# Kernel tuning notes

Hardware: AMD Instinct MI355X
Metric: run time of the kernel (lower is better)

Reference implementation:

```python
import jax, jax.numpy as jnp
import numpy as np

L, V, C, H, T_MAX, FF = 8, 50257, 1024, 16, 1024, 4096
DH = C // H
EPS = 1e-5


def setup_inputs() -> dict:
    key = jax.random.key(0)
    ks = jax.random.split(key, 16)
    s = 0.02
    inp = {
        "idx": jax.random.randint(ks[0], (2, 1024), 0, V, dtype=jnp.int32),
        "tok_emb": jax.random.normal(ks[1], (V, C), jnp.float32) * s,
        "pos_emb": jax.random.normal(ks[2], (T_MAX, C), jnp.float32) * s,
        "qkv_w": jax.random.normal(ks[3], (L, C, 3 * C), jnp.float32) * s,
        "qkv_b": jnp.zeros((L, 3 * C), jnp.float32),
        "out_w": jax.random.normal(ks[4], (L, C, C), jnp.float32) * s,
        "out_b": jnp.zeros((L, C), jnp.float32),
        "ln1_s": jnp.ones((L, C), jnp.float32),
        "ln1_b": jnp.zeros((L, C), jnp.float32),
        "ln2_s": jnp.ones((L, C), jnp.float32),
        "ln2_b": jnp.zeros((L, C), jnp.float32),
        "ffn_w1": jax.random.normal(ks[5], (L, C, FF), jnp.float32) * s,
        "ffn_b1": jnp.zeros((L, FF), jnp.float32),
        "ffn_w2": jax.random.normal(ks[6], (L, FF, C), jnp.float32) * s,
        "ffn_b2": jnp.zeros((L, C), jnp.float32),
        "lnf_s": jnp.ones((C,), jnp.float32),
        "lnf_b": jnp.zeros((C,), jnp.float32),
    }
    return inp


def _layernorm(x, scale, bias):
    m = jnp.mean(x, axis=-1, keepdims=True)
    v = jnp.mean(jnp.square(x - m), axis=-1, keepdims=True)
    return (x - m) * jax.lax.rsqrt(v + EPS) * scale + bias


def reference(idx, tok_emb, pos_emb, qkv_w, qkv_b, out_w, out_b,
              ln1_s, ln1_b, ln2_s, ln2_b,
              ffn_w1, ffn_b1, ffn_w2, ffn_b2, lnf_s, lnf_b):
    B, T = idx.shape
    x = tok_emb[idx] + pos_emb[:T]          # [B,T,C]
    causal = jnp.tril(jnp.ones((T, T), bool))  # [T,T]
    scale = 1.0 / np.sqrt(DH)

    def block(x, p):
        qw, qb, ow, ob, l1s, l1b, l2s, l2b, w1, b1, w2, b2 = p
        h = _layernorm(x, l1s, l1b)
        qkv = h @ qw + qb                    # [B,T,3C]
        q, k, v = jnp.split(qkv, 3, axis=-1)
        q = q.reshape(B, T, H, DH).transpose(0, 2, 1, 3)  # [B,H,T,Dh]
        k = k.reshape(B, T, H, DH).transpose(0, 2, 1, 3)
        v = v.reshape(B, T, H, DH).transpose(0, 2, 1, 3)
        scores = jnp.einsum('bhqd,bhkd->bhqk', q, k) * scale
        scores = jnp.where(causal, scores, -jnp.inf)
        w = jax.nn.softmax(scores, axis=-1)
        o = jnp.einsum('bhqk,bhkd->bhqd', w, v)
        o = o.transpose(0, 2, 1, 3).reshape(B, T, C)
        x = x + (o @ ow + ob)
        h2 = _layernorm(x, l2s, l2b)
        x = x + (jax.nn.gelu(h2 @ w1 + b1, approximate=False) @ w2 + b2)
        return x, None

    params = (qkv_w, qkv_b, out_w, out_b, ln1_s, ln1_b, ln2_s, ln2_b,
              ffn_w1, ffn_b1, ffn_w2, ffn_b2)
    x, _ = jax.lax.scan(block, x, params)
    x = _layernorm(x, lnf_s, lnf_b)
    logits = x @ tok_emb.T                   # tied head, no bias
    return logits
```

## Files before the change

kernel.cpp:

```cpp
#include <hip/hip_runtime.h>
#include <hip/hip_bf16.h>

#define NL 8
#define NV 50257
#define NC 1024
#define NH 16
#define NT 1024
#define NFF 4096
#define NB 2
#define NM (NB*NT)

typedef __attribute__((ext_vector_type(8))) short bf16x8;
typedef __attribute__((ext_vector_type(4))) float f32x4;

__device__ __forceinline__ unsigned short f2bf(float f) {
    union { float f; unsigned u; } a; a.f = f;
    unsigned r = a.u + 0x7FFFu + ((a.u >> 16) & 1u);
    return (unsigned short)(r >> 16);
}

__device__ __forceinline__ void gload16(const unsigned short* g, unsigned short* l) {
    __builtin_amdgcn_global_load_lds(
        (const __attribute__((address_space(1))) unsigned int*)g,
        (__attribute__((address_space(3))) unsigned int*)l,
        16, 0, 0);
}

__global__ __launch_bounds__(256) void embed_kernel(
    const int* __restrict__ idx, const float* __restrict__ te,
    const float* __restrict__ pe, float* __restrict__ x) {
    int row = blockIdx.x;
    int t = row & (NT - 1);
    int id = idx[row];
    const float4 a = reinterpret_cast<const float4*>(te + (size_t)id * NC)[threadIdx.x];
    const float4 b = reinterpret_cast<const float4*>(pe + (size_t)t * NC)[threadIdx.x];
    float4 o; o.x = a.x + b.x; o.y = a.y + b.y; o.z = a.z + b.z; o.w = a.w + b.w;
    reinterpret_cast<float4*>(x + (size_t)row * NC)[threadIdx.x] = o;
}

__global__ __launch_bounds__(256) void cvt_bf16_kernel(
    const float* __restrict__ in, unsigned short* __restrict__ out, size_t n4) {
    size_t i = (size_t)blockIdx.x * 256 + threadIdx.x;
    if (i >= n4) return;
    float4 v = reinterpret_cast<const float4*>(in)[i];
    uint2 u;
    u.x = (unsigned)f2bf(v.x) | ((unsigned)f2bf(v.y) << 16);
    u.y = (unsigned)f2bf(v.z) | ((unsigned)f2bf(v.w) << 16);
    reinterpret_cast<uint2*>(out)[i] = u;
}

__global__ __launch_bounds__(256) void wtrans_kernel(
    const float* __restrict__ W, unsigned short* __restrict__ Wt, int K, int N) {
    __shared__ float tile[32][33];
    int n0 = blockIdx.x * 32, k0 = blockIdx.y * 32;
    int tx = threadIdx.x, ty = threadIdx.y;
#pragma unroll
    for (int i = 0; i < 4; ++i)
        tile[ty + i * 8][tx] = W[(size_t)(k0 + ty + i * 8) * N + n0 + tx];
    __syncthreads();
#pragma unroll
    for (int i = 0; i < 4; ++i)
        Wt[(size_t)(n0 + ty + i * 8) * K + k0 + tx] = f2bf(tile[tx][ty + i * 8]);
}

__global__ __launch_bounds__(256) void ln_kernel(
    const float* __restrict__ x, const float* __restrict__ gam,
    const float* __restrict__ bet, unsigned short* __restrict__ out) {
    __shared__ float red[4];
    int row = blockIdx.x, tid = threadIdx.x;
    const float4 v = reinterpret_cast<const float4*>(x + (size_t)row * NC)[tid];
    float s = v.x + v.y + v.z + v.w;
#pragma unroll
    for (int m = 32; m >= 1; m >>= 1) s += __shfl_xor(s, m, 64);
    if ((tid & 63) == 0) red[tid >> 6] = s;
    __syncthreads();
    float mean = (red[0] + red[1] + red[2] + red[3]) * (1.0f / NC);
    __syncthreads();
    float dx = v.x - mean, dy = v.y - mean, dz = v.z - mean, dw = v.w - mean;
    float q = dx * dx + dy * dy + dz * dz + dw * dw;
#pragma unroll
    for (int m = 32; m >= 1; m >>= 1) q += __shfl_xor(q, m, 64);
    if ((tid & 63) == 0) red[tid >> 6] = q;
    __syncthreads();
    float var = (red[0] + red[1] + red[2] + red[3]) * (1.0f / NC);
    float rstd = rsqrtf(var + 1e-5f);
    int c = tid * 4;
    const float4 g4 = reinterpret_cast<const float4*>(gam)[tid];
    const float4 b4 = reinterpret_cast<const float4*>(bet)[tid];
    uint2 u;
    u.x = (unsigned)f2bf(dx * rstd * g4.x + b4.x) |
          ((unsigned)f2bf(dy * rstd * g4.y + b4.y) << 16);
    u.y = (unsigned)f2bf(dz * rstd * g4.z + b4.z) |
          ((unsigned)f2bf(dw * rstd * g4.w + b4.w) << 16);
    reinterpret_cast<uint2*>(out + (size_t)row * NC + c)[0] = u;
}

template<int ACT, bool BIAS, bool OUTBF16, bool NEDGE, bool ATOMIC>
__global__ __launch_bounds__(256) void gemm_kernel(
    const unsigned short* __restrict__ A, const unsigned short* __restrict__ Bt,
    const float* __restrict__ bias, void* __restrict__ Cout,
    int N, int K, int ldc, int ksub) {
    __shared__ unsigned short As[128 * 32];
    __shared__ unsigned short Bs[128 * 32];
    const int tid = threadIdx.x;
    const int lane = tid & 63;
    const int wave = tid >> 6;
    const int wm = wave >> 1, wn = wave & 1;
    const int lr = lane & 15, lg = lane >> 4;
    const int m0 = blockIdx.x * 128, n0 = blockIdx.y * 128;
    const int kbeg = blockIdx.z * ksub, kend = kbeg + ksub;

    const int r0 = tid >> 2;
    const int c0 = (tid & 3) * 8;
    int bn0 = n0 + r0, bn1 = n0 + r0 + 64;
    if (NEDGE) { bn0 = min(bn0, N - 1); bn1 = min(bn1, N - 1); }
    const unsigned short* Ag0 = A + (size_t)(m0 + r0) * K + c0;
    const unsigned short* Ag1 = A + (size_t)(m0 + r0 + 64) * K + c0;
    const unsigned short* Bg0 = Bt + (size_t)bn0 * K + c0;
    const unsigned short* Bg1 = Bt + (size_t)bn1 * K + c0;
    unsigned short* Al0 = As + wave * 512;
    unsigned short* Al1 = As + 2048 + wave * 512;
    unsigned short* Bl0 = Bs + wave * 512;
    unsigned short* Bl1 = Bs + 2048 + wave * 512;

    const f32x4 zero4 = {0.0f, 0.0f, 0.0f, 0.0f};
    f32x4 acc[4][4];
#pragma unroll
    for (int i = 0; i < 4; ++i)
#pragma unroll
        for (int j = 0; j < 4; ++j) acc[i][j] = zero4;

    for (int k0 = kbeg; k0 < kend; k0 += 32) {
        __syncthreads();
        gload16(Ag0 + k0, Al0);
        gload16(Ag1 + k0, Al1);
        gload16(Bg0 + k0, Bl0);
        gload16(Bg1 + k0, Bl1);
        __syncthreads();
        bf16x8 af[4], bfr[4];
#pragma unroll
        for (int f = 0; f < 4; ++f) {
            af[f]  = *reinterpret_cast<const bf16x8*>(As + (wm * 64 + f * 16 + lr) * 32 + lg * 8);
            bfr[f] = *reinterpret_cast<const bf16x8*>(Bs + (wn * 64 + f * 16 + lr) * 32 + lg * 8);
        }
#pragma unroll
        for (int i = 0; i < 4; ++i)
#pragma unroll
            for (int j = 0; j < 4; ++j)
                acc[i][j] = __builtin_amdgcn_mfma_f32_16x16x32_bf16(af[i], bfr[j], acc[i][j], 0, 0, 0);
    }

#pragma unroll
    for (int i = 0; i < 4; ++i) {
#pragma unroll
        for (int j = 0; j < 4; ++j) {
            int col = n0 + wn * 64 + j * 16 + lr;
            if (NEDGE && col >= N) continue;
            float bv = (BIAS && kbeg == 0) ? bias[col] : 0.0f;
#pragma unroll
            for (int r = 0; r < 4; ++r) {
                int row = m0 + wm * 64 + i * 16 + lg * 4 + r;
                float v = acc[i][j][r] + bv;
                if (ACT == 1) v = 0.5f * v * (1.0f + erff(v * 0.70710678118654752f));
                if (ATOMIC) {
                    atomicAdd(reinterpret_cast<float*>(Cout) + (size_t)row * ldc + col, v);
                } else if (OUTBF16) {
                    reinterpret_cast<unsigned short*>(Cout)[(size_t)row * ldc + col] = f2bf(v);
                } else {
                    reinterpret_cast<float*>(Cout)[(size_t)row * ldc + col] = v;
                }
            }
        }
    }
}

__global__ __launch_bounds__(256) void vtrans_kernel(
    const unsigned short* __restrict__ qkv, unsigned short* __restrict__ vt) {
    __shared__ unsigned short tile[32][33];
    int bh = blockIdx.z; int b = bh >> 4, h = bh & 15;
    int t0 = blockIdx.x * 32, d0 = blockIdx.y * 32;
    int tx = threadIdx.x, ty = threadIdx.y;
#pragma unroll
    for (int i = 0; i < 4; ++i)
        tile[ty + i * 8][tx] =
            qkv[(size_t)(b * NT + t0 + ty + i * 8) * 3072 + 2048 + h * 64 + d0 + tx];
    __syncthreads();
#pragma unroll
    for (int i = 0; i < 4; ++i)
        vt[((size_t)(b * NH + h) * 64 + d0 + ty + i * 8) * NT + t0 + tx] = tile[tx][ty + i * 8];
}

__global__ __launch_bounds__(64) void attn_kernel(
    const unsigned short* __restrict__ qkv, const unsigned short* __restrict__ vt,
    unsigned short* __restrict__ o) {
    __shared__ unsigned short Vs[64][72];
    __shared__ unsigned short Ps[32][72];
    const int qt = blockIdx.x;
    const int h  = blockIdx.y;
    const int b  = blockIdx.z;
    const int lane = threadIdx.x;
    const int lr = lane & 15, lg = lane >> 4;

    const unsigned short* qbase = qkv + (size_t)(b * NT + qt * 32) * 3072 + h * 64;
    bf16x8 qf[2][2];
#pragma unroll
    for (int mf = 0; mf < 2; ++mf)
#pragma unroll
        for (int kc = 0; kc < 2; ++kc)
            qf[mf][kc] = *reinterpret_cast<const bf16x8*>(
                qbase + (size_t)(mf * 16 + lr) * 3072 + kc * 32 + lg * 8);

    const f32x4 zero4 = {0.0f, 0.0f, 0.0f, 0.0f};
    f32x4 oacc[2][4];
    float mrow[2][4], lsum[2][4];
#pragma unroll
    for (int mf = 0; mf < 2; ++mf) {
#pragma unroll
        for (int nf = 0; nf < 4; ++nf) oacc[mf][nf] = zero4;
#pragma unroll
        for (int r = 0; r < 4; ++r) { mrow[mf][r] = -INFINITY; lsum[mf][r] = 0.0f; }
    }

    const int qend = qt * 32 + 32;
    const int nkt = (qend + 63) >> 6;
    const unsigned short* kbase = qkv + (size_t)(b * NT) * 3072 + NC + h * 64;
    const unsigned short* vbase = vt + (size_t)((b * NH + h) * 64) * NT;

    for (int kt = 0; kt < nkt; ++kt) {
        __syncthreads();
#pragma unroll
        for (int i = 0; i < 8; ++i) {
            int chunk = lane + i * 64;
            int d = chunk >> 3;
            int kk = (chunk & 7) * 8;
            *reinterpret_cast<bf16x8*>(&Vs[d][kk]) =
                *reinterpret_cast<const bf16x8*>(vbase + (size_t)d * NT + kt * 64 + kk);
        }
        f32x4 s[2][4];
#pragma unroll
        for (int mf = 0; mf < 2; ++mf)
#pragma unroll
            for (int jf = 0; jf < 4; ++jf) s[mf][jf] = zero4;
#pragma unroll
        for (int kc = 0; kc < 2; ++kc) {
            bf16x8 kf[4];
#pragma unroll
            for (int jf = 0; jf < 4; ++jf)
                kf[jf] = *reinterpret_cast<const bf16x8*>(
                    kbase + (size_t)(kt * 64 + jf * 16 + lr) * 3072 + kc * 32 + lg * 8);
#pragma unroll
            for (int mf = 0; mf < 2; ++mf)
#pragma unroll
                for (int jf = 0; jf < 4; ++jf)
                    s[mf][jf] = __builtin_amdgcn_mfma_f32_16x16x32_bf16(
                        qf[mf][kc], kf[jf], s[mf][jf], 0, 0, 0);
        }
        const bool lastt = (kt == nkt - 1);
#pragma unroll
        for (int mf = 0; mf < 2; ++mf) {
#pragma unroll
            for (int r = 0; r < 4; ++r) {
                int rowg = qt * 32 + mf * 16 + lg * 4 + r;
                float tmax = -INFINITY;
#pragma unroll
                for (int jf = 0; jf < 4; ++jf) {
                    float v = s[mf][jf][r] * 0.125f;
                    if (lastt) {
                        int colg = kt * 64 + jf * 16 + lr;
                        if (colg > rowg) v = -INFINITY;
                    }
                    s[mf][jf][r] = v;
                    tmax = fmaxf(tmax, v);
                }
                tmax = fmaxf(tmax, __shfl_xor(tmax, 1, 64));
                tmax = fmaxf(tmax, __shfl_xor(tmax, 2, 64));
                tmax = fmaxf(tmax, __shfl_xor(tmax, 4, 64));
                tmax = fmaxf(tmax, __shfl_xor(tmax, 8, 64));
                float mnew = fmaxf(mrow[mf][r], tmax);
                float corr = __expf(mrow[mf][r] - mnew);
                float ps = 0.0f;
#pragma unroll
                for (int jf = 0; jf < 4; ++jf) {
                    float p = __expf(s[mf][jf][r] - mnew);
                    s[mf][jf][r] = p;
                    ps += p;
                }
                ps += __shfl_xor(ps, 1, 64);
                ps += __shfl_xor(ps, 2, 64);
                ps += __shfl_xor(ps, 4, 64);
                ps += __shfl_xor(ps, 8, 64);
                lsum[mf][r] = lsum[mf][r] * corr + ps;
                mrow[mf][r] = mnew;
#pragma unroll
                for (int nf = 0; nf < 4; ++nf) oacc[mf][nf][r] *= corr;
            }
        }
#pragma unroll
        for (int mf = 0; mf < 2; ++mf)
#pragma unroll
            for (int jf = 0; jf < 4; ++jf)
#pragma unroll
                for (int r = 0; r < 4; ++r)
                    Ps[mf * 16 + lg * 4 + r][jf * 16 + lr] = f2bf(s[mf][jf][r]);
        __syncthreads();
#pragma unroll
        for (int kc = 0; kc < 2; ++kc) {
            bf16x8 pf[2], vf[4];
#pragma unroll
            for (int mf = 0; mf < 2; ++mf)
                pf[mf] = *reinterpret_cast<const bf16x8*>(&Ps[mf * 16 + lr][kc * 32 + lg * 8]);
#pragma unroll
            for (int nf = 0; nf < 4; ++nf)
                vf[nf] = *reinterpret_cast<const bf16x8*>(&Vs[nf * 16 + lr][kc * 32 + lg * 8]);
#pragma unroll
            for (int mf = 0; mf < 2; ++mf)
#pragma unroll
                for (int nf = 0; nf < 4; ++nf)
                    oacc[mf][nf] = __builtin_amdgcn_mfma_f32_16x16x32_bf16(
                        pf[mf], vf[nf], oacc[mf][nf], 0, 0, 0);
        }
    }

    unsigned short* ob = o + (size_t)(b * NT + qt * 32) * NC + h * 64;
#pragma unroll
    for (int mf = 0; mf < 2; ++mf)
#pragma unroll
        for (int nf = 0; nf < 4; ++nf)
#pragma unroll
            for (int r = 0; r < 4; ++r) {
                float v = oacc[mf][nf][r] / lsum[mf][r];
                ob[(size_t)(mf * 16 + lg * 4 + r) * NC + nf * 16 + lr] = f2bf(v);
            }
}

extern "C" void kernel_launch(void* const* d_in, const int* in_sizes, int n_in,
                              void* d_out, int out_size, void* d_ws, size_t ws_size,
                              hipStream_t stream) {
    (void)in_sizes; (void)n_in; (void)out_size; (void)ws_size;
    const int*   idx    = (const int*)  d_in[0];
    const float* tok    = (const float*)d_in[1];
    const float* pos    = (const float*)d_in[2];
    const float* qkv_w  = (const float*)d_in[3];
    const float* qkv_b  = (const float*)d_in[4];
    const float* out_w  = (const float*)d_in[5];
    const float* out_b  = (const float*)d_in[6];
    const float* ln1_s  = (const float*)d_in[7];
    const float* ln1_b  = (const float*)d_in[8];
    const float* ln2_s  = (const float*)d_in[9];
    const float* ln2_b  = (const float*)d_in[10];
    const float* ffn_w1 = (const float*)d_in[11];
    const float* ffn_b1 = (const float*)d_in[12];
    const float* ffn_w2 = (const float*)d_in[13];
    const float* ffn_b2 = (const float*)d_in[14];
    const float* lnf_s  = (const float*)d_in[15];
    const float* lnf_b  = (const float*)d_in[16];

    char* p = (char*)d_ws;
    float* x              = (float*)p;          p += (size_t)NM * NC * 4;
    unsigned short* hbuf  = (unsigned short*)p; p += (size_t)NM * NC * 2;
    unsigned short* qkvb  = (unsigned short*)p; p += (size_t)NM * 3 * NC * 2;
    unsigned short* obuf  = (unsigned short*)p; p += (size_t)NM * NC * 2;
    unsigned short* gbuf  = (unsigned short*)p; p += (size_t)NM * NFF * 2;
    unsigned short* vtb   = (unsigned short*)p; p += (size_t)NB * NH * 64 * NT * 2;
    unsigned short* wq    = (unsigned short*)p; p += (size_t)3 * NC * NC * 2;
    unsigned short* wo    = (unsigned short*)p; p += (size_t)NC * NC * 2;
    unsigned short* w1    = (unsigned short*)p; p += (size_t)NC * NFF * 2;
    unsigned short* w2    = (unsigned short*)p; p += (size_t)NFF * NC * 2;
    unsigned short* temb  = (unsigned short*)p; p += (size_t)NV * NC * 2;

    {
        size_t n4 = (size_t)NV * NC / 4;
        int blocks = (int)((n4 + 255) / 256);
        cvt_bf16_kernel<<<blocks, 256, 0, stream>>>(tok, temb, n4);
    }
    embed_kernel<<<NM, 256, 0, stream>>>(idx, tok, pos, x);

    for (int l = 0; l < NL; ++l) {
        wtrans_kernel<<<dim3(96, 32),  dim3(32, 8), 0, stream>>>(qkv_w + (size_t)l * NC * 3 * NC, wq, NC, 3 * NC);
        wtrans_kernel<<<dim3(32, 32),  dim3(32, 8), 0, stream>>>(out_w + (size_t)l * NC * NC, wo, NC, NC);
        wtrans_kernel<<<dim3(128, 32), dim3(32, 8), 0, stream>>>(ffn_w1 + (size_t)l * NC * NFF, w1, NC, NFF);
        wtrans_kernel<<<dim3(32, 128), dim3(32, 8), 0, stream>>>(ffn_w2 + (size_t)l * NFF * NC, w2, NFF, NC);

        ln_kernel<<<NM, 256, 0, stream>>>(x, ln1_s + (size_t)l * NC, ln1_b + (size_t)l * NC, hbuf);
        gemm_kernel<0, true, true, false, false><<<dim3(16, 24), 256, 0, stream>>>(
            hbuf, wq, qkv_b + (size_t)l * 3 * NC, qkvb, 3 * NC, NC, 3 * NC, NC);
        vtrans_kernel<<<dim3(32, 2, 32), dim3(32, 8), 0, stream>>>(qkvb, vtb);
        attn_kernel<<<dim3(32, 16, 2), 64, 0, stream>>>(qkvb, vtb, obuf);
        gemm_kernel<0, true, false, false, true><<<dim3(16, 8, 2), 256, 0, stream>>>(
            obuf, wo, out_b + (size_t)l * NC, x, NC, NC, NC, NC / 2);
        ln_kernel<<<NM, 256, 0, stream>>>(x, ln2_s + (size_t)l * NC, ln2_b + (size_t)l * NC, hbuf);
        gemm_kernel<1, true, true, false, false><<<dim3(16, 32), 256, 0, stream>>>(
            hbuf, w1, ffn_b1 + (size_t)l * NFF, gbuf, NFF, NC, NFF, NC);
        gemm_kernel<0, true, false, false, true><<<dim3(16, 8, 4), 256, 0, stream>>>(
            gbuf, w2, ffn_b2 + (size_t)l * NC, x, NC, NFF, NC, NFF / 4);
    }
    ln_kernel<<<NM, 256, 0, stream>>>(x, lnf_s, lnf_b, hbuf);
    gemm_kernel<0, false, false, true, false><<<dim3(16, 393), 256, 0, stream>>>(
        hbuf, temb, nullptr, d_out, NV, NC, NV, NC);
}
```

Baseline: 2.259 ms.

## Add dedicated 256x256-tile pipelined GEMM kernel for the tied LM head

Replaces the generic GEMM for the vocabulary projection with a specialized 512-thread kernel that uses 256x256 output tiles, a multi-slot LDS ring fed by direct global-to-LDS loads with manual vmcnt waits, XOR-swizzled LDS addressing, and grouped block remapping so blocks that run together share tiles. It aims to raise MFMA utilization and data reuse on the largest GEMM (2048x50257x1024). In exchange it carries large register and LDS footprints and hand-written synchronization that could be fragile.

```diff
diff --git a/kernel.cpp b/kernel.cpp
--- a/kernel.cpp
+++ b/kernel.cpp
@@ -24,6 +24,15 @@
         (const __attribute__((address_space(1))) unsigned int*)g,
         (__attribute__((address_space(3))) unsigned int*)l,
         16, 0, 0);
+}
+
+template<int VN> __device__ __forceinline__ void vwait() {
+    asm volatile("s_waitcnt vmcnt(%0)" :: "n"(VN) : "memory");
+}
+__device__ __forceinline__ void barrier_mem() {
+    asm volatile("" ::: "memory");
+    __builtin_amdgcn_s_barrier();
+    asm volatile("" ::: "memory");
 }
 
 __global__ __launch_bounds__(256) void embed_kernel(
@@ -172,6 +181,118 @@
             }
         }
     }
+}
+
+__global__ __launch_bounds__(512, 2) void head_gemm_kernel(
+    const unsigned short* __restrict__ A, const unsigned short* __restrict__ Bt,
+    float* __restrict__ C, int N, int K) {
+    __shared__ unsigned short lds[4][2][8192];
+    const int tid = threadIdx.x;
+    const int lane = tid & 63, wid = tid >> 6;
+    const int wm = wid >> 2, wn = wid & 3;
+    const int lr = lane & 15, lg = lane >> 4;
+
+    const int qx = gridDim.x >> 3;
+    const int orig = blockIdx.x;
+    const int wg = (orig & 7) * qx + (orig >> 3);
+    const int m0 = (wg & 7) * 256;
+    const int n0 = (wg >> 3) * 256;
+
+    const int o0 = tid, o1 = tid + 512;
+    int rA0, kb0, rA1, kb1;
+    { int pr = o0 >> 3, s = o0 & 7; int li = (s << 4) ^ ((pr & 7) << 4);
+      rA0 = (pr << 1) | (li >> 6); kb0 = li & 63; }
+    { int pr = o1 >> 3, s = o1 & 7; int li = (s << 4) ^ ((pr & 7) << 4);
+      rA1 = (pr << 1) | (li >> 6); kb1 = li & 63; }
+    const char* pA0 = (const char*)A + (size_t)(m0 + rA0) * (2 * K) + kb0;
+    const char* pA1 = (const char*)A + (size_t)(m0 + rA1) * (2 * K) + kb1;
+    const char* pB0 = (const char*)Bt + (size_t)min(n0 + rA0, N - 1) * (2 * K) + kb0;
+    const char* pB1 = (const char*)Bt + (size_t)min(n0 + rA1, N - 1) * (2 * K) + kb1;
+    const int dw0 = wid * 512;
+    const int dw1 = 4096 + wid * 512;
+
+    const int swz = (((lr & 1) << 6) | (lg << 4)) ^ (((lr >> 1) & 7) << 4);
+    const int pbA = (wm * 64 + (lr >> 1)) * 128 + swz;
+    const int pbB = (wn * 32 + (lr >> 1)) * 128 + swz;
+
+    auto stage = [&](int slot, int koff) {
+        unsigned short* la = &lds[slot][0][0];
+        unsigned short* lb = &lds[slot][1][0];
+        gload16((const unsigned short*)(pA0 + koff), la + dw0);
+        gload16((const unsigned short*)(pA1 + koff), la + dw1);
+        gload16((const unsigned short*)(pB0 + koff), lb + dw0);
+        gload16((const unsigned short*)(pB1 + koff), lb + dw1);
+    };
+    auto rdA = [&](int slot, int mf) -> bf16x8 {
+        return *reinterpret_cast<const bf16x8*>(
+            (const char*)lds + slot * 32768 + pbA + mf * 1024);
+    };
+    auto rdB = [&](int slot, int nf) -> bf16x8 {
+        return *reinterpret_cast<const bf16x8*>(
+            (const char*)lds + slot * 32768 + 16384 + pbB + nf * 1024);
+    };
+
+    const f32x4 zero4 = {0.0f, 0.0f, 0.0f, 0.0f};
+    f32x4 acc[8][4];
+#pragma unroll
+    for (int i = 0; i < 8; ++i)
+#pragma unroll
+        for (int j = 0; j < 4; ++j) acc[i][j] = zero4;
+
+#define MFMA_ROW(AF, MI) \
+    acc[MI][0] = __builtin_amdgcn_mfma_f32_16x16x32_bf16(AF, bf0, acc[MI][0], 0, 0, 0); \
+    acc[MI][1] = __builtin_amdgcn_mfma_f32_16x16x32_bf16(AF, bf1, acc[MI][1], 0, 0, 0); \
+    acc[MI][2] = __builtin_amdgcn_mfma_f32_16x16x32_bf16(AF, bf2, acc[MI][2], 0, 0, 0); \
+    acc[MI][3] = __builtin_amdgcn_mfma_f32_16x16x32_bf16(AF, bf3, acc[MI][3], 0, 0, 0);
+
+    stage(0, 0);
+    stage(1, 64);
+    const int nk = K >> 6;
+    for (int t = 0; t < nk; ++t) {
+        const int cur = (t & 1) << 1;
+        const int koff = t << 7;
+        const bool pf = (t + 1 < nk);
+        vwait<4>();
+        barrier_mem();
+        if (pf) stage(cur ^ 2, koff + 128);
+        bf16x8 bf0 = rdB(cur, 0), bf1 = rdB(cur, 1), bf2 = rdB(cur, 2), bf3 = rdB(cur, 3);
+        bf16x8 a0 = rdA(cur, 0), a1 = rdA(cur, 1), a2 = rdA(cur, 2), a3 = rdA(cur, 3);
+        __builtin_amdgcn_s_setprio(1);
+        MFMA_ROW(a0, 0) MFMA_ROW(a1, 1) MFMA_ROW(a2, 2) MFMA_ROW(a3, 3)
+        __builtin_amdgcn_s_setprio(0);
+        if (pf) stage((cur ^ 2) | 1, koff + 192);
+        a0 = rdA(cur, 4); a1 = rdA(cur, 5); a2 = rdA(cur, 6); a3 = rdA(cur, 7);
+        __builtin_amdgcn_s_setprio(1);
+        MFMA_ROW(a0, 4) MFMA_ROW(a1, 5) MFMA_ROW(a2, 6) MFMA_ROW(a3, 7)
+        __builtin_amdgcn_s_setprio(0);
+        if (pf) vwait<8>(); else vwait<0>();
+        barrier_mem();
+        const int nxt = cur | 1;
+        bf0 = rdB(nxt, 0); bf1 = rdB(nxt, 1); bf2 = rdB(nxt, 2); bf3 = rdB(nxt, 3);
+        a0 = rdA(nxt, 0); a1 = rdA(nxt, 1); a2 = rdA(nxt, 2); a3 = rdA(nxt, 3);
+        __builtin_amdgcn_s_setprio(1);
+        MFMA_ROW(a0, 0) MFMA_ROW(a1, 1) MFMA_ROW(a2, 2) MFMA_ROW(a3, 3)
+        __builtin_amdgcn_s_setprio(0);
+        a0 = rdA(nxt, 4); a1 = rdA(nxt, 5); a2 = rdA(nxt, 6); a3 = rdA(nxt, 7);
+        __builtin_amdgcn_s_setprio(1);
+        MFMA_ROW(a0, 4) MFMA_ROW(a1, 5) MFMA_ROW(a2, 6) MFMA_ROW(a3, 7)
+        __builtin_amdgcn_s_setprio(0);
+    }
+#undef MFMA_ROW
+
+#pragma unroll
+    for (int mf = 0; mf < 8; ++mf)
+#pragma unroll
+        for (int nf = 0; nf < 4; ++nf) {
+            int col = n0 + wn * 64 + nf * 16 + lr;
+            if (col < N) {
+#pragma unroll
+                for (int r = 0; r < 4; ++r) {
+                    int row = m0 + wm * 128 + mf * 16 + lg * 4 + r;
+                    C[(size_t)row * N + col] = acc[mf][nf][r];
+                }
+            }
+        }
 }
 
 __global__ __launch_bounds__(256) void vtrans_kernel(
@@ -395,6 +516,5 @@
             gbuf, w2, ffn_b2 + (size_t)l * NC, x, NC, NFF, NC, NFF / 4);
     }
     ln_kernel<<<NM, 256, 0, stream>>>(x, lnf_s, lnf_b, hbuf);
-    gemm_kernel<0, false, false, true, false><<<dim3(16, 393), 256, 0, stream>>>(
-        hbuf, temb, nullptr, d_out, NV, NC, NV, NC);
-}
+    head_gemm_kernel<<<dim3(8 * 197), 512, 0, stream>>>(hbuf, temb, (float*)d_out, NV, NC);
+}
```

Measured after the change: 2.220 ms. Within noise of the previous version (-1.7%).
